# Kernel optimization log

Measured on AMD Instinct MI355X. Metric: run time of the kernel, lower is better.

Reference implementation:

```python
import jax, jax.numpy as jnp
import numpy as np

B, S, D, H = 2, 2048, 1024, 16
HD = D // H  # 64
LN_EPS = 1e-5


def setup_inputs() -> dict:
    key = jax.random.key(0)
    ks = jax.random.split(key, 10)
    s = 0.02
    return {
        "x": jax.random.normal(ks[0], (B, S, D), jnp.float32),
        "cdr_bias": jax.random.normal(ks[1], (B, S), jnp.float32),
        "Wq": jax.random.normal(ks[2], (D, D), jnp.float32) * s,
        "bq": jnp.zeros((D,), jnp.float32),
        "Wk": jax.random.normal(ks[3], (D, D), jnp.float32) * s,
        "bk": jnp.zeros((D,), jnp.float32),
        "Wv": jax.random.normal(ks[4], (D, D), jnp.float32) * s,
        "bv": jnp.zeros((D,), jnp.float32),
        "Wo": jax.random.normal(ks[5], (D, D), jnp.float32) * s,
        "bo": jnp.zeros((D,), jnp.float32),
        "gamma": jnp.ones((D,), jnp.float32),
        "beta": jnp.zeros((D,), jnp.float32),
        "cdr_weight": jnp.asarray(1.0, jnp.float32),
    }


def _rotate_half(t):
    # interleaved rotate: [-x2_0, x1_0, -x2_1, x1_1, ...] matching torch stack+reshape
    t1 = t[..., ::2]
    t2 = t[..., 1::2]
    return jnp.stack((-t2, t1), axis=-1).reshape(t.shape)


def reference(x, cdr_bias, Wq, bq, Wk, bk, Wv, bv, Wo, bo, gamma, beta, cdr_weight):
    b, s, d = x.shape

    # RoPE tables (faithful to original: sin/cos concatenated, rotate_half interleaved)
    pos = jnp.arange(s, dtype=x.dtype)
    inv_freq = 1.0 / (10000.0 ** (jnp.arange(0, HD, 2, dtype=x.dtype) / HD))
    sinusoid = pos[:, None] * inv_freq[None, :]              # [S, HD/2]
    sin_pos = jnp.concatenate([jnp.sin(sinusoid)] * 2, -1)   # [S, HD]
    cos_pos = jnp.concatenate([jnp.cos(sinusoid)] * 2, -1)
    sin_pos = sin_pos[None, None]                            # [1,1,S,HD]
    cos_pos = cos_pos[None, None]

    def heads(t):
        return t.reshape(b, s, H, HD).transpose(0, 2, 1, 3)  # [B,H,S,HD]

    Q = heads(x @ Wq + bq)
    K = heads(x @ Wk + bk)
    V = heads(x @ Wv + bv)

    Q = Q * cos_pos + _rotate_half(Q) * sin_pos
    K = K * cos_pos + _rotate_half(K) * sin_pos

    scores = jnp.einsum("bhqd,bhkd->bhqk", Q, K) / jnp.sqrt(jnp.asarray(HD, x.dtype))
    scores = scores + cdr_bias[:, None, None, :] * cdr_weight  # additive key-side bias
    probs = jax.nn.softmax(scores, axis=-1)                    # dropout = identity (eval)

    attn = jnp.einsum("bhqk,bhkd->bhqd", probs, V)
    attn = attn.transpose(0, 2, 1, 3).reshape(b, s, d)
    out = attn @ Wo + bo

    res = x + out
    mu = jnp.mean(res, axis=-1, keepdims=True)
    var = jnp.mean(jnp.square(res - mu), axis=-1, keepdims=True)
    return (res - mu) / jnp.sqrt(var + LN_EPS) * gamma + beta
```

## Files before the change

kernel.cpp:

```cpp
#include <hip/hip_runtime.h>
#include <hip/hip_bf16.h>
#include <math.h>

#define BB 2
#define SS 2048
#define DD 1024
#define HH 16
#define HD 64
#define MM (BB*SS)
#define LN_EPS 1e-5f
#define KVB 64
#define LOG2E 1.44269504088896340736f

typedef unsigned short u16;
typedef unsigned int u32;
typedef __attribute__((ext_vector_type(8))) short short8;
typedef __attribute__((ext_vector_type(4))) float f32x4;
typedef __attribute__((ext_vector_type(4))) unsigned short u16x4;

__device__ __forceinline__ u16 f2bf(float f) {
    union { __hip_bfloat16 h; u16 u; } cv;
    cv.h = __float2bfloat16(f);
    return cv.u;
}
__device__ __forceinline__ float bf2f(u16 u) {
    union { float f; u32 i; } c;
    c.i = (u32)u << 16;
    return c.f;
}

__device__ __forceinline__ float exp2_(float x) {
    float r;
    asm("v_exp_f32 %0, %1" : "=v"(r) : "v"(x));
    return r;
}

__device__ __forceinline__ void gload16(const void* g, void* l) {
    __builtin_amdgcn_global_load_lds(
        (const __attribute__((address_space(1))) void*)g,
        (__attribute__((address_space(3))) void*)l, 16, 0, 0);
}

__global__ __launch_bounds__(256) void k_prep(
        const float* __restrict__ x,
        const float* __restrict__ Wq, const float* __restrict__ Wk,
        const float* __restrict__ Wv, const float* __restrict__ Wo,
        const float* __restrict__ cdr_bias, const float* __restrict__ cw,
        u16* __restrict__ xb, u16* __restrict__ wqkvt, u16* __restrict__ wot,
        float* __restrict__ cosb, float* __restrict__ sinb, float* __restrict__ biasf) {
    __shared__ float t[32][33];
    int bz = blockIdx.x, tid = threadIdx.x;
    if (bz < 4096) {
        int i = bz * 256 + tid;
        float4 v = ((const float4*)x)[i];
        u16x4 o;
        o[0] = f2bf(v.x); o[1] = f2bf(v.y); o[2] = f2bf(v.z); o[3] = f2bf(v.w);
        ((u16x4*)xb)[i] = o;
    } else if (bz < 8192) {
        int zb = bz - 4096;
        int z = zb >> 10, rem = zb & 1023;
        int k0 = (rem & 31) * 32, n0 = (rem >> 5) * 32;
        const float* W = (z == 0) ? Wq : (z == 1) ? Wk : (z == 2) ? Wv : Wo;
        u16* dst = (z < 3) ? (wqkvt + (size_t)z * DD * DD) : wot;
        int tx = tid & 31, ty = tid >> 5;
        #pragma unroll
        for (int r = 0; r < 32; r += 8)
            t[ty + r][tx] = W[(size_t)(k0 + ty + r) * DD + n0 + tx];
        __syncthreads();
        #pragma unroll
        for (int r = 0; r < 32; r += 8)
            dst[(size_t)(n0 + ty + r) * DD + k0 + tx] = f2bf(t[tx][ty + r]);
    } else {
        int idx = (bz - 8192) * 256 + tid;
        if (idx < BB * SS) biasf[idx] = cdr_bias[idx] * cw[0] * LOG2E;
        int s = idx >> 6, j = idx & 63;
        float invf = __powf(10000.0f, -((float)(2 * (j & 31))) / 64.0f);
        float ang = (float)s * invf;
        float sv, cv;
        __sincosf(ang, &sv, &cv);
        cosb[idx] = cv;
        sinb[idx] = sv;
    }
}

#define STAGE_T(A_PTR, B_PTR, T)                                               \
    {                                                                          \
        u16* Ab = Alds + ((T) % 3) * 4096;                                     \
        u16* Bb = Blds + ((T) % 3) * 4096;                                     \
        _Pragma("unroll")                                                      \
        for (int i_ = 0; i_ < 2; i_++) {                                       \
            int p_ = i_ * 256 + tid;                                           \
            int row_ = p_ >> 2, c_ = p_ & 3;                                   \
            gload16(A_PTR + (size_t)(bm + row_) * DD + (T) * 32 + ((c_ ^ (row_ & 3)) << 3), Ab + p_ * 8); \
            gload16(B_PTR + (size_t)(bn + row_) * DD + (T) * 32 + ((c_ ^ (row_ & 3)) << 3), Bb + p_ * 8); \
        }                                                                      \
    }

#define GEMM_PIPE3(A_PTR, B_PTR)                                               \
    f32x4 acc[4][4] = {};                                                      \
    STAGE_T(A_PTR, B_PTR, 0)                                                   \
    STAGE_T(A_PTR, B_PTR, 1)                                                   \
    for (int kt = 0; kt < 32; kt++) {                                          \
        if (kt < 31) asm volatile("s_waitcnt vmcnt(4)" ::: "memory");          \
        else         asm volatile("s_waitcnt vmcnt(0)" ::: "memory");          \
        __builtin_amdgcn_s_barrier();                                          \
        const u16* Acur = Alds + (kt % 3) * 4096;                              \
        const u16* Bcur = Blds + (kt % 3) * 4096;                              \
        short8 a[4], b[4];                                                     \
        int rch = (lg ^ (lr & 3)) << 3;                                        \
        _Pragma("unroll")                                                      \
        for (int i = 0; i < 4; i++) {                                          \
            a[i] = *(const short8*)(Acur + (wm * 64 + i * 16 + lr) * 32 + rch); \
            b[i] = *(const short8*)(Bcur + (wn * 64 + i * 16 + lr) * 32 + rch); \
        }                                                                      \
        if (kt + 2 < 32) STAGE_T(A_PTR, B_PTR, kt + 2)                         \
        __builtin_amdgcn_s_setprio(1);                                         \
        _Pragma("unroll")                                                      \
        for (int i = 0; i < 4; i++)                                            \
            _Pragma("unroll")                                                  \
            for (int j = 0; j < 4; j++)                                        \
                acc[i][j] = __builtin_amdgcn_mfma_f32_16x16x32_bf16(a[i], b[j], acc[i][j], 0, 0, 0); \
        __builtin_amdgcn_s_setprio(0);                                         \
    }                                                                          \
    __syncthreads();

__global__ __launch_bounds__(256, 3) void k_gemm_qkv(
        const u16* __restrict__ xb, const u16* __restrict__ wqkvt,
        const float* __restrict__ bq, const float* __restrict__ bk, const float* __restrict__ bv,
        const float* __restrict__ cosb, const float* __restrict__ sinb,
        u16* __restrict__ q, u16* __restrict__ k, u16* __restrict__ vt) {
    __shared__ u16 SMEM[24576];
    u16* Alds = SMEM;
    u16* Blds = SMEM + 12288;
    int tid = threadIdx.x;
    int lane = tid & 63, wid = tid >> 6;
    int wm = wid >> 1, wn = wid & 1;
    int bm = blockIdx.x * 128, bn = blockIdx.y * 128;
    int lr = lane & 15, lg = lane >> 4;

    GEMM_PIPE3(xb, wqkvt)

    int w = bn >> 10;
    if (w == 2) {
        u16* Tr = SMEM;
        #pragma unroll
        for (int j = 0; j < 4; j++) {
            int n_l = wn * 64 + j * 16 + lr;
            float bias = bv[(bn - 2048) + n_l];
            #pragma unroll
            for (int i = 0; i < 4; i++) {
                ushort4 pk;
                pk.x = f2bf(acc[i][j][0] + bias);
                pk.y = f2bf(acc[i][j][1] + bias);
                pk.z = f2bf(acc[i][j][2] + bias);
                pk.w = f2bf(acc[i][j][3] + bias);
                *(ushort4*)&Tr[n_l * 136 + wm * 64 + i * 16 + lg * 4] = pk;
            }
        }
        __syncthreads();
        int n_r = tid >> 1, hf = tid & 1;
        int nglob = (bn - 2048) + n_r;
        int b_ = bm >> 11;
        size_t vbase = ((size_t)(b_ * HH + (nglob >> 6)) * HD + (nglob & 63)) * SS
                     + (bm & 2047) + hf * 64;
        #pragma unroll
        for (int ii = 0; ii < 8; ii++)
            *(short8*)(vt + vbase + ii * 8) = *(const short8*)&Tr[n_r * 136 + hf * 64 + ii * 8];
    } else {
        int m0 = bm + wm * 64, n0 = bn + wn * 64;
        #pragma unroll
        for (int j = 0; j < 4; j++) {
            int n = n0 + j * 16 + lr;
            int n1 = n & 1023;
            int h = n1 >> 6, d = n1 & 63;
            float bias = (w == 0) ? bq[n1] : bk[n1];
            #pragma unroll
            for (int i = 0; i < 4; i++) {
                #pragma unroll
                for (int r = 0; r < 4; r++) {
                    int m = m0 + i * 16 + lg * 4 + r;
                    int b_ = m >> 11, s = m & 2047;
                    float val = acc[i][j][r] + bias;
                    float part = __shfl_xor(val, 1);
                    float c = cosb[s * 64 + d], sn = sinb[s * 64 + d];
                    float rot = (d & 1) ? part : -part;
                    val = val * c + rot * sn;
                    size_t bh = (size_t)(b_ * HH + h);
                    if (w == 0)
                        q[(bh * SS + s) * HD + d] = f2bf(val * (0.125f * LOG2E));
                    else
                        k[(bh * SS + s) * HD + d] = f2bf(val);
                }
            }
        }
    }
}

__global__ __launch_bounds__(256, 3) void k_gemm_o(
        const u16* __restrict__ attnb, const u16* __restrict__ wot,
        const float* __restrict__ bo, const u16* __restrict__ xb,
        u16* __restrict__ resb) {
    __shared__ u16 SMEM[24576];
    u16* Alds = SMEM;
    u16* Blds = SMEM + 12288;
    int tid = threadIdx.x;
    int lane = tid & 63, wid = tid >> 6;
    int wm = wid >> 1, wn = wid & 1;
    int bm = blockIdx.x * 128, bn = blockIdx.y * 128;
    int lr = lane & 15, lg = lane >> 4;

    GEMM_PIPE3(attnb, wot)

    int m0 = bm + wm * 64, n0 = bn + wn * 64;
    #pragma unroll
    for (int i = 0; i < 4; i++) {
        #pragma unroll
        for (int j = 0; j < 4; j++) {
            int n = n0 + j * 16 + lr;
            float bias = bo[n];
            #pragma unroll
            for (int r = 0; r < 4; r++) {
                int m = m0 + i * 16 + lg * 4 + r;
                float xv = bf2f(xb[(size_t)m * DD + n]);
                resb[(size_t)m * DD + n] = f2bf(acc[i][j][r] + bias + xv);
            }
        }
    }
}

__device__ __forceinline__ void stage64x64(const u16* __restrict__ gbase, size_t rstride,
                                           u16* lds, int tid) {
    int row = tid >> 3, c = tid & 7;
    gload16(gbase + (size_t)row * rstride + (size_t)((c ^ (row & 7)) << 3), lds + tid * 8);
}

__global__ __launch_bounds__(512, 4) void k_attn(
        const u16* __restrict__ q, const u16* __restrict__ kkv, const u16* __restrict__ vt,
        const float* __restrict__ biasf, u16* __restrict__ attnb) {
    __shared__ u16 Klds[2][64 * 64];
    __shared__ u16 Vlds[2][64 * 64];
    __shared__ u16 plds[8][16][72];

    int tid = threadIdx.x;
    int lane = tid & 63, wid = tid >> 6;
    int flat = blockIdx.y * gridDim.x + blockIdx.x;
    int bh = (flat & 7) * 4 + (flat >> 7);
    int qb = (flat >> 3) & 15;
    int b_ = bh >> 4, h = bh & 15;
    int q0 = qb * 128 + wid * 16;
    int lr = lane & 15, lg = lane >> 4;

    short8 qa[2];
    #pragma unroll
    for (int ks = 0; ks < 2; ks++)
        qa[ks] = *(const short8*)(q + ((size_t)bh * SS + q0 + lr) * HD + ks * 32 + lg * 8);

    stage64x64(kkv + ((size_t)bh * SS) * HD, HD, Klds[0], tid);
    stage64x64(vt + ((size_t)bh * HD) * SS, SS, Vlds[0], tid);
    __syncthreads();

    f32x4 acco[4] = {};
    f32x4 acS = {};
    const float* bias_b = biasf + (size_t)b_ * SS;
    short8 vone;
    #pragma unroll
    for (int j = 0; j < 8; j++) vone[j] = (short)0x3F80;

    for (int t = 0; t < SS / KVB; t++) {
        int cur = t & 1;
        if (t + 1 < SS / KVB) {
            int kv1 = (t + 1) * KVB;
            stage64x64(kkv + ((size_t)bh * SS + kv1) * HD, HD, Klds[cur ^ 1], tid);
            stage64x64(vt + ((size_t)bh * HD) * SS + kv1, SS, Vlds[cur ^ 1], tid);
        }
        const u16* Kc = Klds[cur];
        const u16* Vc = Vlds[cur];

        f32x4 s_[4];
        #pragma unroll
        for (int n = 0; n < 4; n++) {
            float4 b4 = *(const float4*)(bias_b + t * KVB + n * 16 + lg * 4);
            s_[n][0] = b4.x; s_[n][1] = b4.y; s_[n][2] = b4.z; s_[n][3] = b4.w;
        }

        short8 kf[4][2], vf[4][2];
        #pragma unroll
        for (int n = 0; n < 4; n++) {
            int row = n * 16 + lr;
            #pragma unroll
            for (int ks = 0; ks < 2; ks++)
                kf[n][ks] = *(const short8*)(Kc + row * 64 + (((ks * 4 + lg) ^ (lr & 7)) << 3));
        }
        #pragma unroll
        for (int dt = 0; dt < 4; dt++) {
            int row = dt * 16 + lr;
            #pragma unroll
            for (int kt = 0; kt < 2; kt++)
                vf[dt][kt] = *(const short8*)(Vc + row * 64 + (((kt * 4 + lg) ^ (lr & 7)) << 3));
        }

        __builtin_amdgcn_s_setprio(1);
        #pragma unroll
        for (int n = 0; n < 4; n++) {
            s_[n] = __builtin_amdgcn_mfma_f32_16x16x32_bf16(kf[n][0], qa[0], s_[n], 0, 0, 0);
            s_[n] = __builtin_amdgcn_mfma_f32_16x16x32_bf16(kf[n][1], qa[1], s_[n], 0, 0, 0);
        }
        __builtin_amdgcn_s_setprio(0);

        #pragma unroll
        for (int n = 0; n < 4; n++) {
            ushort4 pk;
            pk.x = f2bf(exp2_(s_[n][0]));
            pk.y = f2bf(exp2_(s_[n][1]));
            pk.z = f2bf(exp2_(s_[n][2]));
            pk.w = f2bf(exp2_(s_[n][3]));
            *(ushort4*)&plds[wid][lr][n * 16 + lg * 4] = pk;
        }
        asm volatile("s_waitcnt lgkmcnt(0)" ::: "memory");
        __builtin_amdgcn_s_setprio(1);
        #pragma unroll
        for (int kt = 0; kt < 2; kt++) {
            short8 pa = *(const short8*)&plds[wid][lr][kt * 32 + lg * 8];
            #pragma unroll
            for (int dt = 0; dt < 4; dt++)
                acco[dt] = __builtin_amdgcn_mfma_f32_16x16x32_bf16(pa, vf[dt][kt], acco[dt], 0, 0, 0);
            acS = __builtin_amdgcn_mfma_f32_16x16x32_bf16(pa, vone, acS, 0, 0, 0);
        }
        __builtin_amdgcn_s_setprio(0);
        __syncthreads();
    }

    float linv[4];
    #pragma unroll
    for (int r = 0; r < 4; r++) linv[r] = 1.f / acS[r];
    #pragma unroll
    for (int dt = 0; dt < 4; dt++)
        #pragma unroll
        for (int r = 0; r < 4; r++)
            attnb[((size_t)b_ * SS + q0 + lg * 4 + r) * DD + h * HD + dt * 16 + lr] =
                f2bf(acco[dt][r] * linv[r]);
}

__global__ __launch_bounds__(256) void k_ln(const u16* __restrict__ resb,
        const float* __restrict__ gamma, const float* __restrict__ beta,
        float* __restrict__ out) {
    int row = blockIdx.x, tid = threadIdx.x;
    u16x4 v4 = ((const u16x4*)(resb + (size_t)row * DD))[tid];
    float v0 = bf2f(v4[0]), v1 = bf2f(v4[1]), v2 = bf2f(v4[2]), v3 = bf2f(v4[3]);
    float s = v0 + v1 + v2 + v3;
    float ss = v0 * v0 + v1 * v1 + v2 * v2 + v3 * v3;
    #pragma unroll
    for (int off = 32; off; off >>= 1) { s += __shfl_xor(s, off); ss += __shfl_xor(ss, off); }
    __shared__ float sbuf[8];
    int wid = tid >> 6, lane = tid & 63;
    if (lane == 0) { sbuf[wid] = s; sbuf[4 + wid] = ss; }
    __syncthreads();
    s = sbuf[0] + sbuf[1] + sbuf[2] + sbuf[3];
    ss = sbuf[4] + sbuf[5] + sbuf[6] + sbuf[7];
    float mu = s * (1.f / DD);
    float var = ss * (1.f / DD) - mu * mu;
    float rstd = rsqrtf(var + LN_EPS);
    float4 g = ((const float4*)gamma)[tid];
    float4 be = ((const float4*)beta)[tid];
    float4 o;
    o.x = (v0 - mu) * rstd * g.x + be.x;
    o.y = (v1 - mu) * rstd * g.y + be.y;
    o.z = (v2 - mu) * rstd * g.z + be.z;
    o.w = (v3 - mu) * rstd * g.w + be.w;
    ((float4*)(out + (size_t)row * DD))[tid] = o;
}

extern "C" void kernel_launch(void* const* d_in, const int* in_sizes, int n_in,
                              void* d_out, int out_size, void* d_ws, size_t ws_size,
                              hipStream_t stream) {
    const float* x        = (const float*)d_in[0];
    const float* cdr_bias = (const float*)d_in[1];
    const float* Wq       = (const float*)d_in[2];
    const float* bq       = (const float*)d_in[3];
    const float* Wk       = (const float*)d_in[4];
    const float* bk       = (const float*)d_in[5];
    const float* Wv       = (const float*)d_in[6];
    const float* bv       = (const float*)d_in[7];
    const float* Wo       = (const float*)d_in[8];
    const float* bo       = (const float*)d_in[9];
    const float* gamma    = (const float*)d_in[10];
    const float* beta     = (const float*)d_in[11];
    const float* cw       = (const float*)d_in[12];

    char* ws = (char*)d_ws;
    const size_t MB = 1048576;
    u16*   xb     = (u16*)(ws + 0);
    u16*   wqkvt  = (u16*)(ws + 8 * MB);
    u16*   wot    = (u16*)(ws + 14 * MB);
    u16*   qb     = (u16*)(ws + 16 * MB);
    u16*   kb     = (u16*)(ws + 24 * MB);
    u16*   vtb    = (u16*)(ws + 32 * MB);
    u16*   attnb  = (u16*)(ws + 40 * MB);
    u16*   resb   = (u16*)(ws + 48 * MB);
    float* biasf  = (float*)(ws + 48 * MB);
    float* cosb   = (float*)(ws + 64 * MB);
    float* sinb   = (float*)(ws + 64 * MB + 524288);

    k_prep     <<<8704, 256, 0, stream>>>(x, Wq, Wk, Wv, Wo, cdr_bias, cw,
                                          xb, wqkvt, wot, cosb, sinb, biasf);
    k_gemm_qkv <<<dim3(32, 24), 256, 0, stream>>>(xb, wqkvt, bq, bk, bv, cosb, sinb, qb, kb, vtb);
    k_attn     <<<dim3(16, 32), 512, 0, stream>>>(qb, kb, vtb, biasf, attnb);
    k_gemm_o   <<<dim3(32, 8), 256, 0, stream>>>(attnb, wot, bo, xb, resb);
    k_ln       <<<4096, 256, 0, stream>>>(resb, gamma, beta, (float*)d_out);
}
```

Baseline: 120.8 us.

## Split attention KV range across two blocks and add combine kernel

The attention kernel's key/value loop is split into two halves via a third grid dimension. Each half writes unnormalized bf16 partial outputs and fp32 row sums to workspace, and a new combine kernel adds the partials and normalizes them. This doubles the number of attention blocks, giving the GPU more work to spread across compute units. In exchange it adds a kernel launch, extra global memory traffic for the partials, and an extra bf16 rounding of unnormalized accumulators. Workspace regions are reshuffled so the partial buffers overlap buffers that are dead at that point, and the bias buffer moves to a free region.

```diff
diff --git a/kernel.cpp b/kernel.cpp
--- a/kernel.cpp
+++ b/kernel.cpp
@@ -236,7 +236,7 @@
 
 __global__ __launch_bounds__(512, 4) void k_attn(
         const u16* __restrict__ q, const u16* __restrict__ kkv, const u16* __restrict__ vt,
-        const float* __restrict__ biasf, u16* __restrict__ attnb) {
+        const float* __restrict__ biasf, u16* __restrict__ pO, float* __restrict__ pS) {
     __shared__ u16 Klds[2][64 * 64];
     __shared__ u16 Vlds[2][64 * 64];
     __shared__ u16 plds[8][16][72];
@@ -244,19 +244,23 @@
     int tid = threadIdx.x;
     int lane = tid & 63, wid = tid >> 6;
     int flat = blockIdx.y * gridDim.x + blockIdx.x;
+    int split = blockIdx.z;
     int bh = (flat & 7) * 4 + (flat >> 7);
     int qb = (flat >> 3) & 15;
     int b_ = bh >> 4, h = bh & 15;
     int q0 = qb * 128 + wid * 16;
     int lr = lane & 15, lg = lane >> 4;
+    const int T0 = split * 16, T1 = T0 + 16;
 
     short8 qa[2];
     #pragma unroll
     for (int ks = 0; ks < 2; ks++)
         qa[ks] = *(const short8*)(q + ((size_t)bh * SS + q0 + lr) * HD + ks * 32 + lg * 8);
 
-    stage64x64(kkv + ((size_t)bh * SS) * HD, HD, Klds[0], tid);
-    stage64x64(vt + ((size_t)bh * HD) * SS, SS, Vlds[0], tid);
+    const u16* kbase = kkv + (size_t)bh * SS * HD;
+    const u16* vbase = vt + (size_t)bh * HD * SS;
+    stage64x64(kbase + (size_t)T0 * KVB * HD, HD, Klds[0], tid);
+    stage64x64(vbase + T0 * KVB, SS, Vlds[0], tid);
     __syncthreads();
 
     f32x4 acco[4] = {};
@@ -266,12 +270,12 @@
     #pragma unroll
     for (int j = 0; j < 8; j++) vone[j] = (short)0x3F80;
 
-    for (int t = 0; t < SS / KVB; t++) {
+    for (int t = T0; t < T1; t++) {
         int cur = t & 1;
-        if (t + 1 < SS / KVB) {
+        if (t + 1 < T1) {
             int kv1 = (t + 1) * KVB;
-            stage64x64(kkv + ((size_t)bh * SS + kv1) * HD, HD, Klds[cur ^ 1], tid);
-            stage64x64(vt + ((size_t)bh * HD) * SS + kv1, SS, Vlds[cur ^ 1], tid);
+            stage64x64(kbase + (size_t)kv1 * HD, HD, Klds[cur ^ 1], tid);
+            stage64x64(vbase + kv1, SS, Vlds[cur ^ 1], tid);
         }
         const u16* Kc = Klds[cur];
         const u16* Vc = Vlds[cur];
@@ -330,15 +334,33 @@
         __syncthreads();
     }
 
-    float linv[4];
-    #pragma unroll
-    for (int r = 0; r < 4; r++) linv[r] = 1.f / acS[r];
+    size_t poff = (size_t)split * (MM * (size_t)DD);
     #pragma unroll
     for (int dt = 0; dt < 4; dt++)
         #pragma unroll
         for (int r = 0; r < 4; r++)
-            attnb[((size_t)b_ * SS + q0 + lg * 4 + r) * DD + h * HD + dt * 16 + lr] =
-                f2bf(acco[dt][r] * linv[r]);
+            pO[poff + ((size_t)b_ * SS + q0 + lg * 4 + r) * DD + h * HD + dt * 16 + lr] =
+                f2bf(acco[dt][r]);
+    if (lr == 0) {
+        #pragma unroll
+        for (int r = 0; r < 4; r++)
+            pS[split * (32 * SS) + bh * SS + q0 + lg * 4 + r] = acS[r];
+    }
+}
+
+__global__ __launch_bounds__(256) void k_comb(const u16* __restrict__ pO,
+        const float* __restrict__ pS, u16* __restrict__ attnb) {
+    size_t e = ((size_t)blockIdx.x * 256 + threadIdx.x) * 8;
+    int b = (int)(e >> 21), s = (int)((e >> 10) & 2047), h = (int)((e >> 6) & 15);
+    int bhq = (b * HH + h) * SS + s;
+    float inv = 1.f / (pS[bhq] + pS[32 * SS + bhq]);
+    short8 p0 = *(const short8*)(pO + e);
+    short8 p1 = *(const short8*)(pO + (size_t)MM * DD + e);
+    short8 o;
+    #pragma unroll
+    for (int j = 0; j < 8; j++)
+        o[j] = (short)f2bf((bf2f((u16)p0[j]) + bf2f((u16)p1[j])) * inv);
+    *(short8*)(attnb + e) = o;
 }
 
 __global__ __launch_bounds__(256) void k_ln(const u16* __restrict__ resb,
@@ -390,21 +412,24 @@
     char* ws = (char*)d_ws;
     const size_t MB = 1048576;
     u16*   xb     = (u16*)(ws + 0);
+    float* pS     = (float*)(ws + 8 * MB);
     u16*   wqkvt  = (u16*)(ws + 8 * MB);
     u16*   wot    = (u16*)(ws + 14 * MB);
     u16*   qb     = (u16*)(ws + 16 * MB);
     u16*   kb     = (u16*)(ws + 24 * MB);
     u16*   vtb    = (u16*)(ws + 32 * MB);
     u16*   attnb  = (u16*)(ws + 40 * MB);
+    u16*   pO     = (u16*)(ws + 48 * MB);
     u16*   resb   = (u16*)(ws + 48 * MB);
-    float* biasf  = (float*)(ws + 48 * MB);
     float* cosb   = (float*)(ws + 64 * MB);
     float* sinb   = (float*)(ws + 64 * MB + 524288);
+    float* biasf  = (float*)(ws + 65 * MB);
 
     k_prep     <<<8704, 256, 0, stream>>>(x, Wq, Wk, Wv, Wo, cdr_bias, cw,
                                           xb, wqkvt, wot, cosb, sinb, biasf);
     k_gemm_qkv <<<dim3(32, 24), 256, 0, stream>>>(xb, wqkvt, bq, bk, bv, cosb, sinb, qb, kb, vtb);
-    k_attn     <<<dim3(16, 32), 512, 0, stream>>>(qb, kb, vtb, biasf, attnb);
+    k_attn     <<<dim3(16, 32, 2), 512, 0, stream>>>(qb, kb, vtb, biasf, pO, pS);
+    k_comb     <<<2048, 256, 0, stream>>>(pO, pS, attnb);
     k_gemm_o   <<<dim3(32, 8), 256, 0, stream>>>(attnb, wot, bo, xb, resb);
     k_ln       <<<4096, 256, 0, stream>>>(resb, gamma, beta, (float*)d_out);
 }
```

Measured after the change: 127.2 us. +5.3%, slower.
